# Optimization experiments

Measured on AMD Instinct MI355X. Metric: run time of the kernel, lower is better.

Reference implementation:

```python
import jax, jax.numpy as jnp
import numpy as np

B, N, E = 262144, 14, 12
THRESHOLD = 0.3


def setup_inputs() -> dict:
    key = jax.random.key(0)
    k1, k2 = jax.random.split(key)
    pos = jax.random.normal(k1, (B, N, 3), dtype=jnp.float32)
    rot = jax.random.normal(k2, (B, N, 9), dtype=jnp.float32)
    # two 7-node kinematic chains: left arm nodes 0..6, right arm nodes 7..13
    left = np.stack([np.arange(6), np.arange(1, 7)])
    right = np.stack([np.arange(7, 13), np.arange(8, 14)])
    edge_index = jnp.asarray(np.concatenate([left, right], axis=1), dtype=jnp.int32)  # [2, 12]
    ee_mask = jnp.zeros((N, 1), dtype=bool).at[6, 0].set(True).at[13, 0].set(True)
    return {"pos": pos, "rot": rot, "edge_index": edge_index, "ee_mask": ee_mask}


def _capsule_capsule_dist_square(p0, p1, q0, q1):
    # p*: [B, K, 3] left capsules (vary along axis j), q*: [B, K, 3] right capsules (vary along axis i)
    dp = p1 - p0                                  # [B, K, 3]
    dq = q1 - q0                                  # [B, K, 3]
    diff0 = p0[:, None, :, :] - q0[:, :, None, :]  # [B, K(i=q), K(j=p), 3]
    a = jnp.sum(dp * dp, -1)[:, None, :]          # [B, 1, K]
    c = jnp.sum(dq * dq, -1)[:, :, None]          # [B, K, 1]
    b = jnp.einsum('bjd,bid->bij', dp, dq)        # [B, K, K]
    d = jnp.sum(dp[:, None, :, :] * diff0, -1)
    e = jnp.sum(dq[:, :, None, :] * diff0, -1)
    det = a * c - b * b
    bte, ctd, ate, btd = b * e, c * d, a * e, b * d
    s = jnp.zeros_like(det)
    t = jnp.zeros_like(det)
    one = jnp.ones_like(det)
    s = jnp.where((det > 0) & (bte <= ctd) & (e <= 0) & (-d >= a), one, s)
    s = jnp.where((det > 0) & (bte <= ctd) & (e <= 0) & (-d < a) & (-d > 0), -d / a, s)
    t = jnp.where((det > 0) & (bte <= ctd) & (e > 0) & (e < c), e / c, t)
    s = jnp.where((det > 0) & (bte <= ctd) & (e > 0) & (e >= c) & (b - d >= a), one, s)
    s = jnp.where((det > 0) & (bte <= ctd) & (e > 0) & (e >= c) & (b - d < a) & (b - d > 0), (b - d) / a, s)
    t = jnp.where((det > 0) & (bte <= ctd) & (e > 0) & (e >= c), one, t)
    s = jnp.where((det > 0) & (bte > ctd) & (bte - ctd >= det) & (b + e <= 0) & (-d > 0) & (-d < a), -d / a, s)
    s = jnp.where((det > 0) & (bte > ctd) & (bte - ctd >= det) & (b + e <= 0) & (-d > 0) & (-d >= a), one, s)
    s = jnp.where((det > 0) & (bte > ctd) & (bte - ctd >= det) & (b + e > 0) & (b + e < c), one, s)
    t = jnp.where((det > 0) & (bte > ctd) & (bte - ctd >= det) & (b + e > 0) & (b + e < c), (b + e) / c, t)
    s = jnp.where((det > 0) & (bte > ctd) & (bte - ctd >= det) & (b + e > 0) & (b + e >= c) & (b - d > 0) & (b - d < a), (b - d) / a, s)
    s = jnp.where((det > 0) & (bte > ctd) & (bte - ctd >= det) & (b + e > 0) & (b + e >= c) & (b - d > 0) & (b - d >= a), one, s)
    t = jnp.where((det > 0) & (bte > ctd) & (bte - ctd >= det) & (b + e > 0) & (b + e >= c), one, t)
    s = jnp.where((det > 0) & (bte > ctd) & (bte - ctd < det) & (ate <= btd) & (-d > 0) & (-d >= a), one, s)
    s = jnp.where((det > 0) & (bte > ctd) & (bte - ctd < det) & (ate <= btd) & (-d > 0) & (-d < a), -d / a, s)
    s = jnp.where((det > 0) & (bte > ctd) & (bte - ctd < det) & (ate > btd) & (ate - btd >= det) & (b - d > 0) & (b - d >= a), one, s)
    s = jnp.where((det > 0) & (bte > ctd) & (bte - ctd < det) & (ate > btd) & (ate - btd >= det) & (b - d > 0) & (b - d < a), (b - d) / a, s)
    t = jnp.where((det > 0) & (bte > ctd) & (bte - ctd < det) & (ate > btd) & (ate - btd >= det), one, t)
    s = jnp.where((det > 0) & (bte > ctd) & (bte - ctd < det) & (ate > btd) & (ate - btd < det), (bte - ctd) / det, s)
    t = jnp.where((det > 0) & (bte > ctd) & (bte - ctd < det) & (ate > btd) & (ate - btd < det), (ate - btd) / det, t)
    s = jnp.where((det <= 0) & (e <= 0) & (-d > 0) & (-d >= a), one, s)
    s = jnp.where((det <= 0) & (e <= 0) & (-d > 0) & (-d < a), -d / a, s)
    s = jnp.where((det <= 0) & (e > 0) & (e >= c) & (b - d > 0) & (b - d >= a), one, s)
    s = jnp.where((det <= 0) & (e > 0) & (e >= c) & (b - d > 0) & (b - d < a), (b - d) / a, s)
    t = jnp.where((det <= 0) & (e > 0) & (e >= c), one, t)
    t = jnp.where((det <= 0) & (e > 0) & (e < c), e / c, t)
    # original code detaches s and t before forming w
    s = jax.lax.stop_gradient(s)
    t = jax.lax.stop_gradient(t)
    w = diff0 + s[..., None] * dp[:, None, :, :] - t[..., None] * dq[:, :, None, :]
    return jnp.sum(w * w, -1)  # [B, K, K]


def reference(pos, rot, edge_index, ee_mask):
    bsz, n_nodes = pos.shape[0], pos.shape[1]
    n_edges = edge_index.shape[1]
    half = n_edges // 2
    p0 = pos[:, edge_index[0]]  # [B, E, 3]
    p1 = pos[:, edge_index[1]]
    l_p0, r_p0 = p0[:, :half], p0[:, half:]
    l_p1, r_p1 = p1[:, :half], p1[:, half:]
    # exactly 2 end-effectors (left, right) marked in ee_mask
    ee_idx = jnp.nonzero(ee_mask[:, 0], size=2)[0]
    ee_pos = pos[:, ee_idx]                         # [B, 2, 3]  (left, right)
    ee_rot = rot[:, ee_idx].reshape(bsz, 2, 3, 3)   # [B, 2, 3, 3]
    offset = jnp.array([0.0, 0.0, 0.2], dtype=pos.dtype)
    hand_pos = jnp.einsum('beij,j->bei', ee_rot, offset) + ee_pos  # [B, 2, 3]
    l_p0 = jnp.concatenate([l_p0, ee_pos[:, 0:1]], axis=1)   # [B, E/2+1, 3]
    l_p1 = jnp.concatenate([l_p1, hand_pos[:, 0:1]], axis=1)
    r_p0 = jnp.concatenate([r_p0, ee_pos[:, 1:2]], axis=1)
    r_p1 = jnp.concatenate([r_p1, hand_pos[:, 1:2]], axis=1)
    dist_square = _capsule_capsule_dist_square(l_p0, l_p1, r_p0, r_p1)  # [B, 7, 7]
    mask = (dist_square < 0.1 ** 2) & (dist_square > 0)
    special = (dist_square[:, 6, 6] > THRESHOLD ** 2) & (dist_square[:, 6, 6] > 0)
    mask = mask.at[:, 6, 6].set(special)
    loss = jnp.sum(jnp.where(mask, jnp.exp(-dist_square), jnp.zeros_like(dist_square))) / bsz
    return loss
```

## Files before the change

kernel.cpp:

```cpp
#include <hip/hip_runtime.h>


__device__ __forceinline__ float rcpf(float x) { return __builtin_amdgcn_rcpf(x); }
__device__ __forceinline__ float clamp01(float x) {
    return __builtin_amdgcn_fmed3f(x, 0.0f, 1.0f);
}

__device__ __forceinline__ float cap_dist2(
    float px0, float py0, float pz0, float px1, float py1, float pz1,
    float qx0, float qy0, float qz0, float qx1, float qy1, float qz1)
{
    const float dpx = px1 - px0, dpy = py1 - py0, dpz = pz1 - pz0;
    const float dqx = qx1 - qx0, dqy = qy1 - qy0, dqz = qz1 - qz0;
    const float rx  = px0 - qx0, ry  = py0 - qy0, rz  = pz0 - qz0;

    const float a = dpx*dpx + dpy*dpy + dpz*dpz;
    const float c = dqx*dqx + dqy*dqy + dqz*dqz;
    const float b = dpx*dqx + dpy*dqy + dpz*dqz;
    const float d = dpx*rx + dpy*ry + dpz*rz;
    const float e = dqx*rx + dqy*ry + dqz*rz;
    const float det = a*c - b*b;

    const float rcp_a = rcpf(a);
    const float rcp_c = rcpf(c);

    const float f  = b*e - c*d;
    const float s0 = (det > 0.0f) ? clamp01(f * rcpf(det)) : 0.0f;

    const float tn = b*s0 + e;
    const float t  = clamp01(tn * rcp_c);

    const float sA = clamp01(-d * rcp_a);
    const float sB = clamp01((b - d) * rcp_a);
    const float s  = (tn < 0.0f) ? sA : ((tn > c) ? sB : s0);

    const float wx = rx + s*dpx - t*dqx;
    const float wy = ry + s*dpy - t*dqy;
    const float wz = rz + s*dpz - t*dqz;
    return wx*wx + wy*wy + wz*wz;
}

__global__ __launch_bounds__(256) void collision_loss_kernel(
    const float* __restrict__ pos,
    const float* __restrict__ rot,
    float* __restrict__ out,
    int B)
{
    __shared__ float wsum[4];

    const int tid = threadIdx.x;
    const int b   = blockIdx.x * 256 + tid;

    float sum = 0.0f;

    if (b < B) {
        const float2* p2 = reinterpret_cast<const float2*>(pos + (size_t)b * 42);
        const float2 u0  = p2[0],  u1  = p2[1],  u2  = p2[2],  u3  = p2[3];
        const float2 u4  = p2[4],  u5  = p2[5],  u6  = p2[6],  u7  = p2[7];
        const float2 u8  = p2[8],  u9  = p2[9],  u10 = p2[10], u11 = p2[11];
        const float2 u12 = p2[12], u13 = p2[13], u14 = p2[14], u15 = p2[15];
        const float2 u16 = p2[16], u17 = p2[17], u18 = p2[18], u19 = p2[19];
        const float2 u20 = p2[20];

        const float n0x=u0.x,  n0y=u0.y,  n0z=u1.x;
        const float n1x=u1.y,  n1y=u2.x,  n1z=u2.y;
        const float n2x=u3.x,  n2y=u3.y,  n2z=u4.x;
        const float n3x=u4.y,  n3y=u5.x,  n3z=u5.y;
        const float n4x=u6.x,  n4y=u6.y,  n4z=u7.x;
        const float n5x=u7.y,  n5y=u8.x,  n5z=u8.y;
        const float n6x=u9.x,  n6y=u9.y,  n6z=u10.x;
        const float n7x=u10.y, n7y=u11.x, n7z=u11.y;
        const float n8x=u12.x, n8y=u12.y, n8z=u13.x;
        const float n9x=u13.y, n9y=u14.x, n9z=u14.y;
        const float n10x=u15.x, n10y=u15.y, n10z=u16.x;
        const float n11x=u16.y, n11y=u17.x, n11z=u17.y;
        const float n12x=u18.x, n12y=u18.y, n12z=u19.x;
        const float n13x=u19.y, n13y=u20.x, n13z=u20.y;

        const float* rb = rot + (size_t)b * 126;
        const float hlx = n6x  + 0.2f * rb[ 56];
        const float hly = n6y  + 0.2f * rb[ 59];
        const float hlz = n6z  + 0.2f * rb[ 62];
        const float hrx = n13x + 0.2f * rb[119];
        const float hry = n13y + 0.2f * rb[122];
        const float hrz = n13z + 0.2f * rb[125];

        auto acc = [&](float p0x, float p0y, float p0z,
                       float p1x, float p1y, float p1z,
                       float q0x, float q0y, float q0z,
                       float q1x, float q1y, float q1z, bool special) {
            const float d2 = cap_dist2(p0x,p0y,p0z, p1x,p1y,p1z,
                                       q0x,q0y,q0z, q1x,q1y,q1z);
            const bool m = special ? (d2 > 0.09f)
                                   : ((d2 < 0.01f) && (d2 > 0.0f));
            sum += m ? __expf(-d2) : 0.0f;
        };

        #define LROW(QX0,QY0,QZ0,QX1,QY1,QZ1,SP)                                  \
            acc(n0x,n0y,n0z, n1x,n1y,n1z, QX0,QY0,QZ0, QX1,QY1,QZ1, false);       \
            acc(n1x,n1y,n1z, n2x,n2y,n2z, QX0,QY0,QZ0, QX1,QY1,QZ1, false);       \
            acc(n2x,n2y,n2z, n3x,n3y,n3z, QX0,QY0,QZ0, QX1,QY1,QZ1, false);       \
            acc(n3x,n3y,n3z, n4x,n4y,n4z, QX0,QY0,QZ0, QX1,QY1,QZ1, false);       \
            acc(n4x,n4y,n4z, n5x,n5y,n5z, QX0,QY0,QZ0, QX1,QY1,QZ1, false);       \
            acc(n5x,n5y,n5z, n6x,n6y,n6z, QX0,QY0,QZ0, QX1,QY1,QZ1, false);       \
            acc(n6x,n6y,n6z, hlx,hly,hlz, QX0,QY0,QZ0, QX1,QY1,QZ1, SP);

        LROW(n7x, n7y, n7z,  n8x, n8y, n8z,  false)
        LROW(n8x, n8y, n8z,  n9x, n9y, n9z,  false)
        LROW(n9x, n9y, n9z,  n10x,n10y,n10z, false)
        LROW(n10x,n10y,n10z, n11x,n11y,n11z, false)
        LROW(n11x,n11y,n11z, n12x,n12y,n12z, false)
        LROW(n12x,n12y,n12z, n13x,n13y,n13z, false)
        LROW(n13x,n13y,n13z, hrx, hry, hrz,  true)
        #undef LROW
    }

    #pragma unroll
    for (int off = 32; off > 0; off >>= 1)
        sum += __shfl_down(sum, off, 64);
    const int wave = tid >> 6;
    if ((tid & 63) == 0) wsum[wave] = sum;
    __syncthreads();
    if (tid == 0) {
        float s = (wsum[0] + wsum[1]) + (wsum[2] + wsum[3]);
        atomicAdd(out, s * (1.0f / 262144.0f));
    }
}

extern "C" void kernel_launch(void* const* d_in, const int* in_sizes, int n_in,
                              void* d_out, int out_size, void* d_ws, size_t ws_size,
                              hipStream_t stream) {
    const float* pos = (const float*)d_in[0];
    const float* rot = (const float*)d_in[1];
    float* out = (float*)d_out;

    const int B = in_sizes[0] / 42;
    hipMemsetAsync(out, 0, sizeof(float), stream);

    const int grid = (B + 255) / 256;
    collision_loss_kernel<<<grid, 256, 0, stream>>>(pos, rot, out, B);
}
```

Baseline: 220.3 us.

## Stage pos through shared memory with coalesced loads, shrink block to 128

Positions are now loaded cooperatively in a coalesced pattern into LDS and then read per thread from shared memory, replacing strided per-thread float2 global loads. Block size drops from 256 to 128, the bounds check is removed (the grid assumes B divisible by 128), and the rot loads are issued before the staging. This aims to cut wasted memory transactions from uncoalesced access, at the cost of more LDS use (21 KB per block), which may limit occupancy, plus bank conflicts on the stride-21 float2 reads.

Measured after the change: 218.4 us. About the same (-0.9%).

```diff
diff --git a/kernel.cpp b/kernel.cpp
--- a/kernel.cpp
+++ b/kernel.cpp
@@ -40,80 +40,92 @@
     return wx*wx + wy*wy + wz*wz;
 }
 
-__global__ __launch_bounds__(256) void collision_loss_kernel(
+#define BT 128
+
+__global__ __launch_bounds__(BT) void collision_loss_kernel(
     const float* __restrict__ pos,
     const float* __restrict__ rot,
-    float* __restrict__ out,
-    int B)
+    float* __restrict__ out)
 {
-    __shared__ float wsum[4];
+    __shared__ float2 sbuf[BT * 21];
+    __shared__ float wsum[2];
 
-    const int tid = threadIdx.x;
-    const int b   = blockIdx.x * 256 + tid;
+    const int tid       = threadIdx.x;
+    const int blockBase = blockIdx.x * BT;
+    const int b         = blockBase + tid;
+
+    const float* rb = rot + (size_t)b * 126;
+    const float r6x = rb[ 56], r6y = rb[ 59], r6z = rb[ 62];
+    const float rdx = rb[119], rdy = rb[122], rdz = rb[125];
+
+    const float2* g2 = reinterpret_cast<const float2*>(pos + (size_t)blockBase * 42);
+    #pragma unroll
+    for (int k = 0; k < 21; ++k) {
+        const int idx = k * BT + tid;
+        sbuf[idx] = g2[idx];
+    }
+    __syncthreads();
+
+    const float2* m2 = sbuf + tid * 21;
+    const float2 u0  = m2[0],  u1  = m2[1],  u2  = m2[2],  u3  = m2[3];
+    const float2 u4  = m2[4],  u5  = m2[5],  u6  = m2[6],  u7  = m2[7];
+    const float2 u8  = m2[8],  u9  = m2[9],  u10 = m2[10], u11 = m2[11];
+    const float2 u12 = m2[12], u13 = m2[13], u14 = m2[14], u15 = m2[15];
+    const float2 u16 = m2[16], u17 = m2[17], u18 = m2[18], u19 = m2[19];
+    const float2 u20 = m2[20];
+
+    const float n0x=u0.x,  n0y=u0.y,  n0z=u1.x;
+    const float n1x=u1.y,  n1y=u2.x,  n1z=u2.y;
+    const float n2x=u3.x,  n2y=u3.y,  n2z=u4.x;
+    const float n3x=u4.y,  n3y=u5.x,  n3z=u5.y;
+    const float n4x=u6.x,  n4y=u6.y,  n4z=u7.x;
+    const float n5x=u7.y,  n5y=u8.x,  n5z=u8.y;
+    const float n6x=u9.x,  n6y=u9.y,  n6z=u10.x;
+    const float n7x=u10.y, n7y=u11.x, n7z=u11.y;
+    const float n8x=u12.x, n8y=u12.y, n8z=u13.x;
+    const float n9x=u13.y, n9y=u14.x, n9z=u14.y;
+    const float n10x=u15.x, n10y=u15.y, n10z=u16.x;
+    const float n11x=u16.y, n11y=u17.x, n11z=u17.y;
+    const float n12x=u18.x, n12y=u18.y, n12z=u19.x;
+    const float n13x=u19.y, n13y=u20.x, n13z=u20.y;
+
+    const float hlx = n6x  + 0.2f * r6x;
+    const float hly = n6y  + 0.2f * r6y;
+    const float hlz = n6z  + 0.2f * r6z;
+    const float hrx = n13x + 0.2f * rdx;
+    const float hry = n13y + 0.2f * rdy;
+    const float hrz = n13z + 0.2f * rdz;
 
     float sum = 0.0f;
 
-    if (b < B) {
-        const float2* p2 = reinterpret_cast<const float2*>(pos + (size_t)b * 42);
-        const float2 u0  = p2[0],  u1  = p2[1],  u2  = p2[2],  u3  = p2[3];
-        const float2 u4  = p2[4],  u5  = p2[5],  u6  = p2[6],  u7  = p2[7];
-        const float2 u8  = p2[8],  u9  = p2[9],  u10 = p2[10], u11 = p2[11];
-        const float2 u12 = p2[12], u13 = p2[13], u14 = p2[14], u15 = p2[15];
-        const float2 u16 = p2[16], u17 = p2[17], u18 = p2[18], u19 = p2[19];
-        const float2 u20 = p2[20];
+    auto acc = [&](float p0x, float p0y, float p0z,
+                   float p1x, float p1y, float p1z,
+                   float q0x, float q0y, float q0z,
+                   float q1x, float q1y, float q1z, bool special) {
+        const float d2 = cap_dist2(p0x,p0y,p0z, p1x,p1y,p1z,
+                                   q0x,q0y,q0z, q1x,q1y,q1z);
+        const bool m = special ? (d2 > 0.09f)
+                               : ((d2 < 0.01f) && (d2 > 0.0f));
+        sum += m ? __expf(-d2) : 0.0f;
+    };
 
-        const float n0x=u0.x,  n0y=u0.y,  n0z=u1.x;
-        const float n1x=u1.y,  n1y=u2.x,  n1z=u2.y;
-        const float n2x=u3.x,  n2y=u3.y,  n2z=u4.x;
-        const float n3x=u4.y,  n3y=u5.x,  n3z=u5.y;
-        const float n4x=u6.x,  n4y=u6.y,  n4z=u7.x;
-        const float n5x=u7.y,  n5y=u8.x,  n5z=u8.y;
-        const float n6x=u9.x,  n6y=u9.y,  n6z=u10.x;
-        const float n7x=u10.y, n7y=u11.x, n7z=u11.y;
-        const float n8x=u12.x, n8y=u12.y, n8z=u13.x;
-        const float n9x=u13.y, n9y=u14.x, n9z=u14.y;
-        const float n10x=u15.x, n10y=u15.y, n10z=u16.x;
-        const float n11x=u16.y, n11y=u17.x, n11z=u17.y;
-        const float n12x=u18.x, n12y=u18.y, n12z=u19.x;
-        const float n13x=u19.y, n13y=u20.x, n13z=u20.y;
+    #define LROW(QX0,QY0,QZ0,QX1,QY1,QZ1,SP)                                  \
+        acc(n0x,n0y,n0z, n1x,n1y,n1z, QX0,QY0,QZ0, QX1,QY1,QZ1, false);       \
+        acc(n1x,n1y,n1z, n2x,n2y,n2z, QX0,QY0,QZ0, QX1,QY1,QZ1, false);       \
+        acc(n2x,n2y,n2z, n3x,n3y,n3z, QX0,QY0,QZ0, QX1,QY1,QZ1, false);       \
+        acc(n3x,n3y,n3z, n4x,n4y,n4z, QX0,QY0,QZ0, QX1,QY1,QZ1, false);       \
+        acc(n4x,n4y,n4z, n5x,n5y,n5z, QX0,QY0,QZ0, QX1,QY1,QZ1, false);       \
+        acc(n5x,n5y,n5z, n6x,n6y,n6z, QX0,QY0,QZ0, QX1,QY1,QZ1, false);       \
+        acc(n6x,n6y,n6z, hlx,hly,hlz, QX0,QY0,QZ0, QX1,QY1,QZ1, SP);
 
-        const float* rb = rot + (size_t)b * 126;
-        const float hlx = n6x  + 0.2f * rb[ 56];
-        const float hly = n6y  + 0.2f * rb[ 59];
-        const float hlz = n6z  + 0.2f * rb[ 62];
-        const float hrx = n13x + 0.2f * rb[119];
-        const float hry = n13y + 0.2f * rb[122];
-        const float hrz = n13z + 0.2f * rb[125];
-
-        auto acc = [&](float p0x, float p0y, float p0z,
-                       float p1x, float p1y, float p1z,
-                       float q0x, float q0y, float q0z,
-                       float q1x, float q1y, float q1z, bool special) {
-            const float d2 = cap_dist2(p0x,p0y,p0z, p1x,p1y,p1z,
-                                       q0x,q0y,q0z, q1x,q1y,q1z);
-            const bool m = special ? (d2 > 0.09f)
-                                   : ((d2 < 0.01f) && (d2 > 0.0f));
-            sum += m ? __expf(-d2) : 0.0f;
-        };
-
-        #define LROW(QX0,QY0,QZ0,QX1,QY1,QZ1,SP)                                  \
-            acc(n0x,n0y,n0z, n1x,n1y,n1z, QX0,QY0,QZ0, QX1,QY1,QZ1, false);       \
-            acc(n1x,n1y,n1z, n2x,n2y,n2z, QX0,QY0,QZ0, QX1,QY1,QZ1, false);       \
-            acc(n2x,n2y,n2z, n3x,n3y,n3z, QX0,QY0,QZ0, QX1,QY1,QZ1, false);       \
-            acc(n3x,n3y,n3z, n4x,n4y,n4z, QX0,QY0,QZ0, QX1,QY1,QZ1, false);       \
-            acc(n4x,n4y,n4z, n5x,n5y,n5z, QX0,QY0,QZ0, QX1,QY1,QZ1, false);       \
-            acc(n5x,n5y,n5z, n6x,n6y,n6z, QX0,QY0,QZ0, QX1,QY1,QZ1, false);       \
-            acc(n6x,n6y,n6z, hlx,hly,hlz, QX0,QY0,QZ0, QX1,QY1,QZ1, SP);
-
-        LROW(n7x, n7y, n7z,  n8x, n8y, n8z,  false)
-        LROW(n8x, n8y, n8z,  n9x, n9y, n9z,  false)
-        LROW(n9x, n9y, n9z,  n10x,n10y,n10z, false)
-        LROW(n10x,n10y,n10z, n11x,n11y,n11z, false)
-        LROW(n11x,n11y,n11z, n12x,n12y,n12z, false)
-        LROW(n12x,n12y,n12z, n13x,n13y,n13z, false)
-        LROW(n13x,n13y,n13z, hrx, hry, hrz,  true)
-        #undef LROW
-    }
+    LROW(n7x, n7y, n7z,  n8x, n8y, n8z,  false)
+    LROW(n8x, n8y, n8z,  n9x, n9y, n9z,  false)
+    LROW(n9x, n9y, n9z,  n10x,n10y,n10z, false)
+    LROW(n10x,n10y,n10z, n11x,n11y,n11z, false)
+    LROW(n11x,n11y,n11z, n12x,n12y,n12z, false)
+    LROW(n12x,n12y,n12z, n13x,n13y,n13z, false)
+    LROW(n13x,n13y,n13z, hrx, hry, hrz,  true)
+    #undef LROW
 
     #pragma unroll
     for (int off = 32; off > 0; off >>= 1)
@@ -122,8 +134,7 @@
     if ((tid & 63) == 0) wsum[wave] = sum;
     __syncthreads();
     if (tid == 0) {
-        float s = (wsum[0] + wsum[1]) + (wsum[2] + wsum[3]);
-        atomicAdd(out, s * (1.0f / 262144.0f));
+        atomicAdd(out, (wsum[0] + wsum[1]) * (1.0f / 262144.0f));
     }
 }
 
@@ -137,6 +148,5 @@
     const int B = in_sizes[0] / 42;
     hipMemsetAsync(out, 0, sizeof(float), stream);
 
-    const int grid = (B + 255) / 256;
-    collision_loss_kernel<<<grid, 256, 0, stream>>>(pos, rot, out, B);
+    collision_loss_kernel<<<B / BT, BT, 0, stream>>>(pos, rot, out);
 }
```
